# Performance work log

Measured on AMD Instinct MI355X. Metric: run time of the kernel, lower is better.

Reference implementation:

```python
import jax, jax.numpy as jnp
import numpy as np

B, T, F, H = 64, 128, 188, 16  # batch, time, in_features, feature_embed_dim
N_CONT = F - 11  # features 11.. are continuous (177)


def setup_inputs() -> dict:
    key = jax.random.key(0)
    ks = jax.random.split(key, 14)
    s = 1.0 / np.sqrt(H)  # nn.Linear default init scale
    u = lambda k, shape: jax.random.uniform(k, shape, jnp.float32, -s, s)
    return {
        "x": jax.random.normal(ks[0], (B, T, F * H), jnp.float32),
        # grouped per-feature Linear weights, grouped by output dim
        "W2a": u(ks[1], (4, H, 2)),  "b2a": u(ks[2], (4, 2)),   # features 0-3
        "W3":  u(ks[3], (2, H, 3)),  "b3":  u(ks[4], (2, 3)),   # features 4-5
        "W4":  u(ks[5], (1, H, 4)),  "b4":  u(ks[6], (1, 4)),   # feature 6
        "W6":  u(ks[7], (1, H, 6)),  "b6":  u(ks[8], (1, 6)),   # feature 7
        "W7":  u(ks[9], (3, H, 7)),  "b7":  u(ks[10], (3, 7)),  # features 8-10
        "Wc":  u(ks[11], (N_CONT, H, 2)), "bc": u(ks[12], (N_CONT, 2)),  # features 11..
        "eps": jax.random.normal(ks[13], (B * T, N_CONT), jnp.float32),  # normal-sampling noise
    }


def _cat_argmax(xg, W, b):
    # softmax then argmax == argmax of logits
    logits = jnp.einsum('nfd,fdo->nfo', xg, W) + b
    return jnp.argmax(logits, axis=-1).astype(jnp.float32)


def reference(x, W2a, b2a, W3, b3, W4, b4, W6, b6, W7, b7, Wc, bc, eps):
    xr = x.reshape(B * T, F, H)
    cats = jnp.concatenate([
        _cat_argmax(xr[:, 0:4],  W2a, b2a),
        _cat_argmax(xr[:, 4:6],  W3,  b3),
        _cat_argmax(xr[:, 6:7],  W4,  b4),
        _cat_argmax(xr[:, 7:8],  W6,  b6),
        _cat_argmax(xr[:, 8:11], W7,  b7),
    ], axis=1)  # [N, 11]
    dec = jnp.einsum('nfd,fdo->nfo', xr[:, 11:], Wc) + bc  # [N, 177, 2]
    mean = jnp.tanh(dec[..., 0])
    std = jax.nn.sigmoid(dec[..., 1])
    samp = mean + std * eps  # reparameterized t.normal(mean, std)
    outs = jnp.concatenate([cats, samp], axis=1)  # [N, 188]
    return outs.reshape(B, T, F)
```

## Files before the change

kernel.cpp:

```cpp
#include <hip/hip_runtime.h>
#include <hip/hip_bf16.h>
#include <cmath>

#define NROWS   8192
#define FDIM    188
#define HDIM    16
#define NCONT   177
#define XSTRIDE 3008
#define CFPAD   178

#define CAT_TOTAL 765

__global__ __launch_bounds__(256)
void tab_dec_kernel(const float* __restrict__ x,
                    const float* __restrict__ W2a, const float* __restrict__ b2a,
                    const float* __restrict__ W3,  const float* __restrict__ b3,
                    const float* __restrict__ W4,  const float* __restrict__ b4,
                    const float* __restrict__ W6,  const float* __restrict__ b6,
                    const float* __restrict__ W7,  const float* __restrict__ b7,
                    const float* __restrict__ Wc,  const float* __restrict__ bc,
                    const float* __restrict__ eps,
                    float* __restrict__ out)
{
    __shared__ float sWcT[32 * CFPAD];
    __shared__ float sbcT[2 * CFPAD];
    __shared__ float sCat[CAT_TOTAL];

    const int tid = threadIdx.x;

    for (int i = tid; i < NCONT * 32; i += 256) {
        int cf = i >> 5;
        int c  = i & 31;
        sWcT[c * CFPAD + cf] = Wc[i];
    }
    for (int i = tid; i < NCONT * 2; i += 256) {
        int cf = i >> 1;
        int o  = i & 1;
        sbcT[o * CFPAD + cf] = bc[i];
    }
    for (int i = tid; i < 128; i += 256) sCat[i]       = W2a[i];
    for (int i = tid; i <  96; i += 256) sCat[128 + i] = W3[i];
    for (int i = tid; i <  64; i += 256) sCat[224 + i] = W4[i];
    for (int i = tid; i <  96; i += 256) sCat[288 + i] = W6[i];
    for (int i = tid; i < 336; i += 256) sCat[384 + i] = W7[i];
    if (tid <  8) sCat[720 + tid] = b2a[tid];
    if (tid <  6) sCat[728 + tid] = b3[tid];
    if (tid <  4) sCat[734 + tid] = b4[tid];
    if (tid <  6) sCat[738 + tid] = b6[tid];
    if (tid < 21) sCat[744 + tid] = b7[tid];
    __syncthreads();

    const int total  = NROWS * FDIM;
    const int stride = gridDim.x * blockDim.x;

    for (int idx = blockIdx.x * blockDim.x + tid; idx < total; idx += stride) {
        const int n = idx / FDIM;
        const int f = idx - n * FDIM;

        const float4* xp = reinterpret_cast<const float4*>(
            x + (size_t)n * XSTRIDE + (size_t)f * HDIM);
        float4 v0 = xp[0], v1 = xp[1], v2 = xp[2], v3 = xp[3];
        float xv[16] = { v0.x, v0.y, v0.z, v0.w,
                         v1.x, v1.y, v1.z, v1.w,
                         v2.x, v2.y, v2.z, v2.w,
                         v3.x, v3.y, v3.z, v3.w };

        float res;
        if (f >= 11) {
            const int cf = f - 11;
            float m  = sbcT[cf];
            float sg = sbcT[CFPAD + cf];
            #pragma unroll
            for (int d = 0; d < 16; ++d) {
                m  = fmaf(xv[d], sWcT[(2 * d)     * CFPAD + cf], m);
                sg = fmaf(xv[d], sWcT[(2 * d + 1) * CFPAD + cf], sg);
            }
            const float mean = tanhf(m);
            const float stdv = 1.0f / (1.0f + __expf(-sg));
            res = fmaf(stdv, eps[(size_t)n * NCONT + cf], mean);
        } else {
            int g, wo, bo, odim;
            if (f < 4)      { g = f;     wo = 0;   bo = 720; odim = 2; }
            else if (f < 6) { g = f - 4; wo = 128; bo = 728; odim = 3; }
            else if (f < 7) { g = 0;     wo = 224; bo = 734; odim = 4; }
            else if (f < 8) { g = 0;     wo = 288; bo = 738; odim = 6; }
            else            { g = f - 8; wo = 384; bo = 744; odim = 7; }
            const float* W = sCat + wo + g * HDIM * odim;
            const float* bb = sCat + bo + g * odim;
            float best = -1e30f;
            int   bi   = 0;
            for (int o = 0; o < odim; ++o) {
                float acc = bb[o];
                #pragma unroll
                for (int d = 0; d < 16; ++d) acc = fmaf(xv[d], W[d * odim + o], acc);
                if (acc > best) { best = acc; bi = o; }
            }
            res = (float)bi;
        }
        out[idx] = res;
    }
}

extern "C" void kernel_launch(void* const* d_in, const int* in_sizes, int n_in,
                              void* d_out, int out_size, void* d_ws, size_t ws_size,
                              hipStream_t stream) {
    const float* x   = (const float*)d_in[0];
    const float* W2a = (const float*)d_in[1];
    const float* b2a = (const float*)d_in[2];
    const float* W3  = (const float*)d_in[3];
    const float* b3  = (const float*)d_in[4];
    const float* W4  = (const float*)d_in[5];
    const float* b4  = (const float*)d_in[6];
    const float* W6  = (const float*)d_in[7];
    const float* b6  = (const float*)d_in[8];
    const float* W7  = (const float*)d_in[9];
    const float* b7  = (const float*)d_in[10];
    const float* Wc  = (const float*)d_in[11];
    const float* bc  = (const float*)d_in[12];
    const float* eps = (const float*)d_in[13];
    float* out = (float*)d_out;

    dim3 grid(1280), block(256);
    hipLaunchKernelGGL(tab_dec_kernel, grid, block, 0, stream,
                       x, W2a, b2a, W3, b3, W4, b4, W6, b6, W7, b7, Wc, bc, eps, out);
}
```

Baseline: 180.4 us.

## Assign each thread one feature over a chunk of rows, weights in registers

```diff
diff --git a/kernel.cpp b/kernel.cpp
--- a/kernel.cpp
+++ b/kernel.cpp
@@ -6,10 +6,11 @@
 #define FDIM    188
 #define HDIM    16
 #define NCONT   177
+#define NCAT    11
 #define XSTRIDE 3008
-#define CFPAD   178
+#define CHUNK   8
+#define NB      (NROWS / CHUNK)
 
-#define CAT_TOTAL 765
 
 __global__ __launch_bounds__(256)
 void tab_dec_kernel(const float* __restrict__ x,
@@ -22,71 +23,70 @@
                     const float* __restrict__ eps,
                     float* __restrict__ out)
 {
-    __shared__ float sWcT[32 * CFPAD];
-    __shared__ float sbcT[2 * CFPAD];
-    __shared__ float sCat[CAT_TOTAL];
+    const int t  = blockIdx.x * blockDim.x + threadIdx.x;
+    const int TC = NCONT * NB;
 
-    const int tid = threadIdx.x;
+    if (t < TC) {
+        const int nb = t / NCONT;
+        const int cf = t - nb * NCONT;
 
-    for (int i = tid; i < NCONT * 32; i += 256) {
-        int cf = i >> 5;
-        int c  = i & 31;
-        sWcT[c * CFPAD + cf] = Wc[i];
-    }
-    for (int i = tid; i < NCONT * 2; i += 256) {
-        int cf = i >> 1;
-        int o  = i & 1;
-        sbcT[o * CFPAD + cf] = bc[i];
-    }
-    for (int i = tid; i < 128; i += 256) sCat[i]       = W2a[i];
-    for (int i = tid; i <  96; i += 256) sCat[128 + i] = W3[i];
-    for (int i = tid; i <  64; i += 256) sCat[224 + i] = W4[i];
-    for (int i = tid; i <  96; i += 256) sCat[288 + i] = W6[i];
-    for (int i = tid; i < 336; i += 256) sCat[384 + i] = W7[i];
-    if (tid <  8) sCat[720 + tid] = b2a[tid];
-    if (tid <  6) sCat[728 + tid] = b3[tid];
-    if (tid <  4) sCat[734 + tid] = b4[tid];
-    if (tid <  6) sCat[738 + tid] = b6[tid];
-    if (tid < 21) sCat[744 + tid] = b7[tid];
-    __syncthreads();
+        float w[32];
+        const float4* wp = reinterpret_cast<const float4*>(Wc + cf * 32);
+        #pragma unroll
+        for (int k = 0; k < 8; ++k) {
+            float4 v = wp[k];
+            w[4*k+0] = v.x; w[4*k+1] = v.y; w[4*k+2] = v.z; w[4*k+3] = v.w;
+        }
+        const float b0 = bc[cf * 2 + 0];
+        const float b1 = bc[cf * 2 + 1];
 
-    const int total  = NROWS * FDIM;
-    const int stride = gridDim.x * blockDim.x;
+        const int n0 = nb * CHUNK;
+        const float* xbase = x + (size_t)n0 * XSTRIDE + (size_t)(NCAT + cf) * HDIM;
 
-    for (int idx = blockIdx.x * blockDim.x + tid; idx < total; idx += stride) {
-        const int n = idx / FDIM;
-        const int f = idx - n * FDIM;
-
-        const float4* xp = reinterpret_cast<const float4*>(
-            x + (size_t)n * XSTRIDE + (size_t)f * HDIM);
-        float4 v0 = xp[0], v1 = xp[1], v2 = xp[2], v3 = xp[3];
-        float xv[16] = { v0.x, v0.y, v0.z, v0.w,
-                         v1.x, v1.y, v1.z, v1.w,
-                         v2.x, v2.y, v2.z, v2.w,
-                         v3.x, v3.y, v3.z, v3.w };
-
-        float res;
-        if (f >= 11) {
-            const int cf = f - 11;
-            float m  = sbcT[cf];
-            float sg = sbcT[CFPAD + cf];
+        #pragma unroll 2
+        for (int j = 0; j < CHUNK; ++j) {
+            const float4* xq = reinterpret_cast<const float4*>(xbase + (size_t)j * XSTRIDE);
+            float4 a0 = xq[0], a1 = xq[1], a2 = xq[2], a3 = xq[3];
+            float xv[16] = { a0.x, a0.y, a0.z, a0.w,
+                             a1.x, a1.y, a1.z, a1.w,
+                             a2.x, a2.y, a2.z, a2.w,
+                             a3.x, a3.y, a3.z, a3.w };
+            float m = b0, s = b1;
             #pragma unroll
             for (int d = 0; d < 16; ++d) {
-                m  = fmaf(xv[d], sWcT[(2 * d)     * CFPAD + cf], m);
-                sg = fmaf(xv[d], sWcT[(2 * d + 1) * CFPAD + cf], sg);
+                m = fmaf(xv[d], w[2*d],     m);
+                s = fmaf(xv[d], w[2*d + 1], s);
             }
-            const float mean = tanhf(m);
-            const float stdv = 1.0f / (1.0f + __expf(-sg));
-            res = fmaf(stdv, eps[(size_t)n * NCONT + cf], mean);
-        } else {
-            int g, wo, bo, odim;
-            if (f < 4)      { g = f;     wo = 0;   bo = 720; odim = 2; }
-            else if (f < 6) { g = f - 4; wo = 128; bo = 728; odim = 3; }
-            else if (f < 7) { g = 0;     wo = 224; bo = 734; odim = 4; }
-            else if (f < 8) { g = 0;     wo = 288; bo = 738; odim = 6; }
-            else            { g = f - 8; wo = 384; bo = 744; odim = 7; }
-            const float* W = sCat + wo + g * HDIM * odim;
-            const float* bb = sCat + bo + g * odim;
+            float mc   = fminf(fmaxf(m, -10.0f), 10.0f);
+            float mean = 1.0f - 2.0f / (__expf(2.0f * mc) + 1.0f);
+            float stdv = 1.0f / (1.0f + __expf(-s));
+            const int n = n0 + j;
+            out[(size_t)n * FDIM + NCAT + cf] =
+                fmaf(stdv, eps[(size_t)n * NCONT + cf], mean);
+        }
+    } else if (t < TC + NCAT * NB) {
+        const int tt = t - TC;
+        const int nb = tt / NCAT;
+        const int f  = tt - nb * NCAT;
+
+        const float *W, *bb;
+        int odim;
+        if (f < 4)      { W = W2a + f * HDIM * 2;      bb = b2a + f * 2; odim = 2; }
+        else if (f < 6) { W = W3 + (f - 4) * HDIM * 3; bb = b3 + (f - 4) * 3; odim = 3; }
+        else if (f < 7) { W = W4;                      bb = b4;          odim = 4; }
+        else if (f < 8) { W = W6;                      bb = b6;          odim = 6; }
+        else            { W = W7 + (f - 8) * HDIM * 7; bb = b7 + (f - 8) * 7; odim = 7; }
+
+        const int n0 = nb * CHUNK;
+        for (int j = 0; j < CHUNK; ++j) {
+            const int n = n0 + j;
+            const float4* xq = reinterpret_cast<const float4*>(
+                x + (size_t)n * XSTRIDE + (size_t)f * HDIM);
+            float4 a0 = xq[0], a1 = xq[1], a2 = xq[2], a3 = xq[3];
+            float xv[16] = { a0.x, a0.y, a0.z, a0.w,
+                             a1.x, a1.y, a1.z, a1.w,
+                             a2.x, a2.y, a2.z, a2.w,
+                             a3.x, a3.y, a3.z, a3.w };
             float best = -1e30f;
             int   bi   = 0;
             for (int o = 0; o < odim; ++o) {
@@ -95,9 +95,8 @@
                 for (int d = 0; d < 16; ++d) acc = fmaf(xv[d], W[d * odim + o], acc);
                 if (acc > best) { best = acc; bi = o; }
             }
-            res = (float)bi;
+            out[(size_t)n * FDIM + f] = (float)bi;
         }
-        out[idx] = res;
     }
 }
 
@@ -120,7 +119,8 @@
     const float* eps = (const float*)d_in[13];
     float* out = (float*)d_out;
 
-    dim3 grid(1280), block(256);
+    const int total_threads = (NCONT + NCAT) * NB;
+    dim3 grid((total_threads + 255) / 256), block(256);
     hipLaunchKernelGGL(tab_dec_kernel, grid, block, 0, stream,
                        x, W2a, b2a, W3, b3, W4, b4, W6, b6, W7, b7, Wc, bc, eps, out);
 }
```

Result: slower. 208.3 us (+15.5%).
